# Performance work log

Hardware: AMD Instinct MI355X
Metric: run time of the kernel (lower is better)

The kernel has to match this reference:

```python
import jax, jax.numpy as jnp
import numpy as np

NSAMPLE = 16   # knn neighbors for cost volume
KCLUST = 8     # cluster size stand-in for custom_cluster_pc1 (min_count=8)
B, N, D = 2, 4096, 64


def _sqdist(src, dst):
    # src [B,N,C], dst [B,M,C] -> [B,N,M]
    d = (jnp.sum(src * src, -1)[:, :, None]
         + jnp.sum(dst * dst, -1)[:, None, :]
         - 2.0 * jnp.einsum('bnc,bmc->bnm', src, dst))
    return jnp.maximum(d, 0.0)


def _knn(k, xyz, new_xyz):
    return jax.lax.top_k(-_sqdist(new_xyz, xyz), k)[1]  # [B,S,k] indices of k smallest


def _group(points, idx):
    # points [B,M,C], idx [B,N,K] -> [B,N,K,C]
    b = jnp.arange(points.shape[0])[:, None, None]
    return points[b, idx]


def _weightnet(x, w1, b1, w2, b2, w3, b3):
    # x [B,N,K,3]; 1x1 conv stack == per-point MLP, relu
    h = jax.nn.relu(jnp.einsum('bnkc,cd->bnkd', x, w1) + b1)
    h = jax.nn.relu(jnp.einsum('bnkc,cd->bnkd', h, w2) + b2)
    return jax.nn.relu(jnp.einsum('bnkc,cd->bnkd', h, w3) + b3)


def _leaky(x):
    return jnp.where(x > 0, x, 0.1 * x)


def _forward(xyz1, xyz2, points1, points2, vel1, vel2, mask1, mask2,
             w_xyz, w_vel, w_points,
             mlp_w1, mlp_b1, mlp_w2, mlp_b2,
             wn1_w1, wn1_b1, wn1_w2, wn1_b2, wn1_w3, wn1_b3,
             wn2_w1, wn2_b1, wn2_w2, wn2_b2, wn2_w3, wn2_b3):
    xyz1t = jnp.transpose(xyz1, (0, 2, 1))      # [B,N1,3]
    xyz2t = jnp.transpose(xyz2, (0, 2, 1))      # [B,N2,3]
    p1t = jnp.transpose(points1, (0, 2, 1))     # [B,N1,D1]
    p2t = jnp.transpose(points2, (0, 2, 1))     # [B,N2,D2]

    # --- custom_cluster_pc1 stand-in: knn clusters of pc1 with its velocities ---
    idx_c = _knn(KCLUST, xyz1t, xyz1t)                     # [B,N,KC]
    cc = _group(xyz1t, idx_c)                              # [B,N,KC,3]
    cv = _group(vel1[..., None], idx_c)[..., 0]            # [B,N,KC]

    u = cc / jnp.linalg.norm(cc, axis=-1, keepdims=True)
    ATA = jnp.einsum('bnki,bnkj->bnij', u, u) + 1e-6 * jnp.eye(3, dtype=u.dtype)
    ATb = jnp.einsum('bnki,bnk->bni', u, cv)
    v_world = jnp.linalg.solve(ATA, ATb[..., None])[..., 0]  # [B,N,3]

    # --- feature-space knn between weighted (xyz, points) concatenations ---
    f1 = jnp.concatenate([w_xyz * xyz1t, w_points * p1t], axis=-1)
    f2 = jnp.concatenate([w_xyz * xyz2t, w_points * p2t], axis=-1)
    knn_idx = _knn(NSAMPLE, f2, f1)                        # [B,N1,K]

    neighbor_xyz = _group(xyz2t, knn_idx)                  # [B,N1,K,3]
    direction_xyz = neighbor_xyz - xyz1t[:, :, None, :]
    g2 = _group(p2t, knn_idx)                              # [B,N1,K,D2]
    g1 = jnp.broadcast_to(p1t[:, :, None, :], g2.shape[:3] + (p1t.shape[-1],))
    new_points = jnp.concatenate([g1, g2, direction_xyz], axis=-1)  # [B,N1,K,D1+D2+3]

    h = _leaky(jnp.einsum('bnkc,cd->bnkd', new_points, mlp_w1) + mlp_b1)
    h = _leaky(jnp.einsum('bnkc,cd->bnkd', h, mlp_w2) + mlp_b2)    # [B,N1,K,128]

    w = _weightnet(direction_xyz, wn1_w1, wn1_b1, wn1_w2, wn1_b2, wn1_w3, wn1_b3)
    point_to_patch = jnp.sum(w * h, axis=2)                # [B,N1,128]

    # --- second grouping in rigid-velocity space ---
    idx2 = _knn(NSAMPLE, v_world, v_world)
    nxyz1 = _group(xyz1t, idx2)
    dir2 = nxyz1 - xyz1t[:, :, None, :]
    w2 = _weightnet(dir2, wn2_w1, wn2_b1, wn2_w2, wn2_b2, wn2_w3, wn2_b3)
    gcost = _group(point_to_patch, idx2)                   # [B,N1,K,128]
    patch_to_patch = jnp.sum(w2 * gcost, axis=2)           # [B,N1,128]

    return jnp.transpose(patch_to_patch, (0, 2, 1)), v_world  # [B,128,N1], [B,N1,3]


def setup_inputs() -> dict:
    key = jax.random.key(0)
    ks = jax.random.split(key, 24)
    s = 0.05
    inp = {
        'xyz1': jax.random.normal(ks[0], (B, 3, N), jnp.float32),
        'xyz2': jax.random.normal(ks[1], (B, 3, N), jnp.float32),
        'points1': jax.random.normal(ks[2], (B, D, N), jnp.float32),
        'points2': jax.random.normal(ks[3], (B, D, N), jnp.float32),
        'vel1': jax.random.normal(ks[4], (B, N), jnp.float32),
        'vel2': jax.random.normal(ks[5], (B, N), jnp.float32),
        'mask1': jnp.ones((B, N), jnp.float32),
        'mask2': jnp.ones((B, N), jnp.float32),
        'w_xyz': jnp.float32(0.4), 'w_vel': jnp.float32(0.2), 'w_points': jnp.float32(0.4),
        'mlp_w1': jax.random.normal(ks[6], (2 * D + 3, 128), jnp.float32) * s,
        'mlp_b1': jnp.zeros((128,), jnp.float32),
        'mlp_w2': jax.random.normal(ks[7], (128, 128), jnp.float32) * s,
        'mlp_b2': jnp.zeros((128,), jnp.float32),
    }
    for tag, base in (('wn1', 8), ('wn2', 14)):
        inp[f'{tag}_w1'] = jax.random.normal(ks[base], (3, 8), jnp.float32) * s
        inp[f'{tag}_b1'] = jnp.zeros((8,), jnp.float32)
        inp[f'{tag}_w2'] = jax.random.normal(ks[base + 1], (8, 8), jnp.float32) * s
        inp[f'{tag}_b2'] = jnp.zeros((8,), jnp.float32)
        inp[f'{tag}_w3'] = jax.random.normal(ks[base + 2], (8, 128), jnp.float32) * s
        inp[f'{tag}_b3'] = jnp.zeros((128,), jnp.float32)
    return inp


def reference(xyz1, xyz2, points1, points2, vel1, vel2, mask1, mask2,
              w_xyz, w_vel, w_points,
              mlp_w1, mlp_b1, mlp_w2, mlp_b2,
              wn1_w1, wn1_b1, wn1_w2, wn1_b2, wn1_w3, wn1_b3,
              wn2_w1, wn2_b1, wn2_w2, wn2_b2, wn2_w3, wn2_b3):
    return _forward(xyz1, xyz2, points1, points2, vel1, vel2, mask1, mask2,
                    w_xyz, w_vel, w_points,
                    mlp_w1, mlp_b1, mlp_w2, mlp_b2,
                    wn1_w1, wn1_b1, wn1_w2, wn1_b2, wn1_w3, wn1_b3,
                    wn2_w1, wn2_b1, wn2_w2, wn2_b2, wn2_w3, wn2_b3)
```

## Files before the change

### kernel.cpp

```cpp
#include <hip/hip_runtime.h>

#define NPTS 4096
#define NQ   8192
#define DD   64
#define KNN  16
#define KC   8
#define NSEG 16
#define SEGLEN 256
#define KB96 96
#define VOFF 1048576

#define ALWAYS_INLINE __attribute__((always_inline)) inline

typedef __attribute__((ext_vector_type(8))) short bf16x8;
typedef __attribute__((ext_vector_type(4))) float f32x4;

__device__ ALWAYS_INLINE float leakyf(float x) { return x > 0.f ? x : 0.1f * x; }

__device__ ALWAYS_INLINE unsigned short bf16rne(float f) {
  unsigned u = __float_as_uint(f);
  u = (u + 0x7FFFu + ((u >> 16) & 1u)) >> 16;
  return (unsigned short)u;
}

__device__ ALWAYS_INLINE float packdt(float d, unsigned tag12) {
  return __uint_as_float((__float_as_uint(d) & 0xFFFFF000u) | tag12);
}

#define TK8_FOREACH(M)  M(0) M(1) M(2) M(3) M(4) M(5) M(6) M(7)
#define TK16_FOREACH(M) M(0) M(1) M(2) M(3) M(4) M(5) M(6) M(7) \
                        M(8) M(9) M(10) M(11) M(12) M(13) M(14) M(15)

#define TK_DECL1(i) float tkd##i = 3.4e38f; int tki##i = 0;
#define TK_STEP1(i) { bool c = vd < tkd##i; float t_ = tkd##i; int u_ = tki##i; \
                      tkd##i = c ? vd : tkd##i; tki##i = c ? vi : tki##i; \
                      vd = c ? t_ : vd; vi = c ? u_ : vi; }
#define TK8_DECL  TK8_FOREACH(TK_DECL1)
#define TK8_INS(dexp, mexp)  { float vd = (dexp); int vi = (mexp); \
                               if (vd < tkd7)  { TK8_FOREACH(TK_STEP1) } }

#define PK_DECL1(i) float pk##i = __uint_as_float(0x7F7FFFFFu);
#define PK_STEP1(i) { float lo_ = fminf(pk##i, pv); pv = fmaxf(pk##i, pv); pk##i = lo_; }
#define PK16_DECL    TK16_FOREACH(PK_DECL1)
#define PK16_INS(ve) { float pv = (ve); TK16_FOREACH(PK_STEP1) }
#define PK_STORE1(i) pdq[i] = pk##i;
#define PK16_STORE   TK16_FOREACH(PK_STORE1)

__global__ __launch_bounds__(256) void k_prep(
    const float* __restrict__ xyz1, const float* __restrict__ xyz2,
    const float* __restrict__ pts1, const float* __restrict__ pts2,
    const float* __restrict__ w_xyz_p, const float* __restrict__ w_points_p,
    unsigned short* __restrict__ f1b, unsigned short* __restrict__ f2b,
    float* __restrict__ n1, float* __restrict__ n2a,
    float* __restrict__ p1t, float* __restrict__ p2t,
    float* __restrict__ x1t, float* __restrict__ x2t)
{
  int gid = blockIdx.x * 256 + threadIdx.x;
  int b = gid >> 12, n = gid & (NPTS - 1);
  float wx = w_xyz_p[0], wp = w_points_p[0];
  {
    const float* xb = xyz1 + (size_t)b * 3 * NPTS;
    float x = xb[n], y = xb[NPTS + n], z = xb[2 * NPTS + n];
    float nrm2 = fmaf(z, z, fmaf(y, y, x * x));
    float4 xv; xv.x = x; xv.y = y; xv.z = z; xv.w = nrm2;
    *(float4*)&x1t[(size_t)gid * 4] = xv;
    float fx = wx * x, fy = wx * y, fz = wx * z;
    float acc = fmaf(fz, fz, fmaf(fy, fy, fx * fx));
    unsigned short* fr = f1b + (size_t)gid * KB96;
    fr[0] = bf16rne(fx); fr[1] = bf16rne(fy); fr[2] = bf16rne(fz);
    const float* pb = pts1 + (size_t)b * DD * NPTS;
    float* pr = p1t + (size_t)gid * DD;
    for (int c = 0; c < DD; ++c) {
      float v = pb[(size_t)c * NPTS + n];
      pr[c] = v;
      float fv = wp * v;
      fr[3 + c] = bf16rne(fv);
      acc = fmaf(fv, fv, acc);
    }
    for (int c = 67; c < KB96; ++c) fr[c] = 0;
    n1[gid] = acc;
  }
  {
    const float* xb = xyz2 + (size_t)b * 3 * NPTS;
    float x = xb[n], y = xb[NPTS + n], z = xb[2 * NPTS + n];
    float nrm2 = fmaf(z, z, fmaf(y, y, x * x));
    float4 xv; xv.x = x; xv.y = y; xv.z = z; xv.w = nrm2;
    *(float4*)&x2t[(size_t)gid * 4] = xv;
    float fx = wx * x, fy = wx * y, fz = wx * z;
    float acc = fmaf(fz, fz, fmaf(fy, fy, fx * fx));
    unsigned short* fr = f2b + (size_t)gid * KB96;
    fr[0] = bf16rne(fx); fr[1] = bf16rne(fy); fr[2] = bf16rne(fz);
    const float* pb = pts2 + (size_t)b * DD * NPTS;
    float* pr = p2t + (size_t)gid * DD;
    for (int c = 0; c < DD; ++c) {
      float v = pb[(size_t)c * NPTS + n];
      pr[c] = v;
      float fv = wp * v;
      fr[3 + c] = bf16rne(fv);
      acc = fmaf(fv, fv, acc);
    }
    for (int c = 67; c < KB96; ++c) fr[c] = 0;
    n2a[gid] = acc;
  }
}

__global__ __launch_bounds__(256) void k_knn3(
    const float* __restrict__ x4, float* __restrict__ pd, int* __restrict__ pi)
{
  __shared__ __align__(16) float4 sc[128];
  int seg = blockIdx.y;
  int Q = blockIdx.x * 256 + threadIdx.x;
  int b = Q >> 12;
  float4 q = *(const float4*)&x4[(size_t)Q * 4];
  TK8_DECL
  int gbase = (b << 12) + seg * SEGLEN;
  for (int ch = 0; ch < SEGLEN / 128; ++ch) {
    __syncthreads();
    if (threadIdx.x < 128)
      sc[threadIdx.x] = *(const float4*)&x4[(size_t)(gbase + ch * 128 + threadIdx.x) * 4];
    __syncthreads();
    int m0 = seg * SEGLEN + ch * 128;
    for (int j = 0; j < 128; ++j) {
      float4 c = sc[j];
      float dot = fmaf(q.z, c.z, fmaf(q.y, c.y, q.x * c.x));
      float d = fmaxf(q.w + c.w - 2.f * dot, 0.f);
      TK8_INS(d, m0 + j)
    }
  }
  float* pdq = pd + ((size_t)Q * NSEG + seg) * 16;
  int* piq = pi + ((size_t)Q * NSEG + seg) * 16;
#define ST8(i) pdq[i] = tkd##i; piq[i] = tki##i;
  TK8_FOREACH(ST8)
#undef ST8
}

__global__ __launch_bounds__(256) void k_knnv(
    const float* __restrict__ x4, float* __restrict__ pd)
{
  __shared__ __align__(16) float4 sc[128];
  int seg = blockIdx.y;
  int Q = blockIdx.x * 256 + threadIdx.x;
  int b = Q >> 12;
  float4 q = *(const float4*)&x4[(size_t)Q * 4];
  PK16_DECL
  int gbase = (b << 12) + seg * SEGLEN;
  for (int ch = 0; ch < SEGLEN / 128; ++ch) {
    __syncthreads();
    if (threadIdx.x < 128)
      sc[threadIdx.x] = *(const float4*)&x4[(size_t)(gbase + ch * 128 + threadIdx.x) * 4];
    __syncthreads();
    unsigned base_tag = ((unsigned)ch << 11) | (unsigned)seg;
#pragma unroll
    for (int j = 0; j < 128; ++j) {
      float4 c = sc[j];
      float dot = fmaf(q.z, c.z, fmaf(q.y, c.y, q.x * c.x));
      float d = fmaxf(q.w + c.w - 2.f * dot, 0.f);
      PK16_INS(packdt(d, base_tag | ((unsigned)j << 4)))
    }
  }
  float* pdq = pd + ((size_t)Q * NSEG + seg) * 16;
  PK16_STORE
}

__global__ __launch_bounds__(256) void k_rigid(
    const float* __restrict__ pd, const int* __restrict__ pi,
    const float* __restrict__ x4, const float* __restrict__ vel1,
    float* __restrict__ vout, float* __restrict__ v4out)
{
  int Q = blockIdx.x * 256 + threadIdx.x;
  int b = Q >> 12;
  TK8_DECL
  for (int s = 0; s < NSEG; ++s) {
    const float* pdq = pd + ((size_t)Q * NSEG + s) * 16;
    const int* piq = pi + ((size_t)Q * NSEG + s) * 16;
#pragma unroll
    for (int j = 0; j < KC; ++j) TK8_INS(pdq[j], piq[j])
  }
  int base = b << 12;
  double a00 = 0, a01 = 0, a02 = 0, a11 = 0, a12 = 0, a22 = 0;
  double r0 = 0, r1 = 0, r2 = 0;
#define RIG_ACC(i) { \
    float4 c = *(const float4*)&x4[(size_t)(base + tki##i) * 4]; \
    float nr = sqrtf(c.w); \
    float ux = c.x / nr, uy = c.y / nr, uz = c.z / nr; \
    float cv = vel1[base + tki##i]; \
    double dx = ux, dy = uy, dz = uz, dvv = cv; \
    a00 += dx * dx; a01 += dx * dy; a02 += dx * dz; \
    a11 += dy * dy; a12 += dy * dz; a22 += dz * dz; \
    r0 += dx * dvv; r1 += dy * dvv; r2 += dz * dvv; }
  TK8_FOREACH(RIG_ACC)
#undef RIG_ACC
  a00 += 1e-6; a11 += 1e-6; a22 += 1e-6;
  double c00 = a11 * a22 - a12 * a12;
  double c01 = a02 * a12 - a01 * a22;
  double c02 = a01 * a12 - a02 * a11;
  double c11 = a00 * a22 - a02 * a02;
  double c12 = a02 * a01 - a00 * a12;
  double c22 = a00 * a11 - a01 * a01;
  double det = a00 * c00 + a01 * c01 + a02 * c02;
  double inv = 1.0 / det;
  float vx = (float)((c00 * r0 + c01 * r1 + c02 * r2) * inv);
  float vy = (float)((c01 * r0 + c11 * r1 + c12 * r2) * inv);
  float vz = (float)((c02 * r0 + c12 * r1 + c22 * r2) * inv);
  vout[(size_t)Q * 3 + 0] = vx;
  vout[(size_t)Q * 3 + 1] = vy;
  vout[(size_t)Q * 3 + 2] = vz;
  float4 v; v.x = vx; v.y = vy; v.z = vz;
  v.w = fmaf(vz, vz, fmaf(vy, vy, vx * vx));
  *(float4*)&v4out[(size_t)Q * 4] = v;
}

__global__ __launch_bounds__(256) void k_knnf_mfma(
    const unsigned short* __restrict__ f1b, const unsigned short* __restrict__ f2b,
    const float* __restrict__ n1, const float* __restrict__ n2a,
    float* __restrict__ pd)
{
  __shared__ __align__(16) unsigned short sf1[16 * KB96];
  __shared__ __align__(16) unsigned short sf2[64 * KB96];
  __shared__ __align__(16) float sn1[16];
  __shared__ __align__(16) float sn2[64];
  __shared__ __align__(16) float sD[64][21];
  int tid = threadIdx.x;
  int w = tid >> 6, lane = tid & 63;
  int i15 = lane & 15, g = lane >> 4, kr0 = g * 8;
  int blockq = blockIdx.x * 16;
  int b = blockq >> 12;
  int seg = blockIdx.y;
  int gbase = (b << 12) + seg * 1024;
  {
    const float4* src = (const float4*)(f1b + (size_t)blockq * KB96);
    if (tid < 192) ((float4*)sf1)[tid] = src[tid];
    if (tid < 16) sn1[tid] = n1[blockq + tid];
  }
  __syncthreads();
  bf16x8 af0 = *(const bf16x8*)&sf1[i15 * KB96 + kr0];
  bf16x8 af1 = *(const bf16x8*)&sf1[i15 * KB96 + 32 + kr0];
  bf16x8 af2 = *(const bf16x8*)&sf1[i15 * KB96 + 64 + kr0];
  float nq0 = sn1[g * 4 + 0], nq1 = sn1[g * 4 + 1];
  float nq2 = sn1[g * 4 + 2], nq3 = sn1[g * 4 + 3];
  PK16_DECL
  int q_tk = tid & 15, p_tk = tid >> 4;
  for (int ch = 0; ch < 16; ++ch) {
    __syncthreads();
    {
      const float4* src = (const float4*)(f2b + (size_t)(gbase + ch * 64) * KB96);
      ((float4*)sf2)[tid] = src[tid];
      ((float4*)sf2)[tid + 256] = src[tid + 256];
      ((float4*)sf2)[tid + 512] = src[tid + 512];
      if (tid < 64) sn2[tid] = n2a[gbase + ch * 64 + tid];
    }
    __syncthreads();
    {
      int crow = w * 16 + i15;
      const unsigned short* c_ = &sf2[crow * KB96 + kr0];
      f32x4 acc = {0.f, 0.f, 0.f, 0.f};
      acc = __builtin_amdgcn_mfma_f32_16x16x32_bf16(af0, *(const bf16x8*)&c_[0],  acc, 0, 0, 0);
      acc = __builtin_amdgcn_mfma_f32_16x16x32_bf16(af1, *(const bf16x8*)&c_[32], acc, 0, 0, 0);
      acc = __builtin_amdgcn_mfma_f32_16x16x32_bf16(af2, *(const bf16x8*)&c_[64], acc, 0, 0, 0);
      float nn2 = sn2[crow];
      unsigned tag = (((unsigned)(ch * 16 + i15)) << 4) | (unsigned)(seg * 4 + w);
      sD[crow][g * 4 + 0] = packdt(fmaxf(nq0 + nn2 - 2.f * acc[0], 0.f), tag);
      sD[crow][g * 4 + 1] = packdt(fmaxf(nq1 + nn2 - 2.f * acc[1], 0.f), tag);
      sD[crow][g * 4 + 2] = packdt(fmaxf(nq2 + nn2 - 2.f * acc[2], 0.f), tag);
      sD[crow][g * 4 + 3] = packdt(fmaxf(nq3 + nn2 - 2.f * acc[3], 0.f), tag);
    }
    __syncthreads();
    if (tid < 64) {
#pragma unroll
      for (int cl = 0; cl < 16; ++cl)
        PK16_INS(sD[p_tk * 16 + cl][q_tk])
    }
  }
  if (tid < 64) {
    int pseg = seg * 4 + p_tk;
    float* pdq = pd + ((size_t)(blockq + q_tk) * NSEG + pseg) * 16;
    PK16_STORE
  }
}

template<int MODE>
__global__ __launch_bounds__(256) void k_mergepk(
    const float* __restrict__ pd, int* __restrict__ oidx)
{
  int Q = blockIdx.x * 256 + threadIdx.x;
  PK16_DECL
  for (int s = 0; s < NSEG; ++s) {
    const float* pdq = pd + ((size_t)Q * NSEG + s) * 16;
    for (int j = 0; j < 16; ++j) {
      float v = pdq[j];
      if (__all(!(v < pk15))) break;
      PK16_INS(v)
    }
  }
#define DEC(i) { unsigned u = __float_as_uint(pk##i); int m_; \
    if (MODE == 0) { unsigned ps = u & 15u, lo = (u >> 4) & 255u; \
      m_ = (int)(((ps >> 2) << 10) + ((lo >> 4) << 6) + ((ps & 3u) << 4) + (lo & 15u)); } \
    else { m_ = (int)(((u & 15u) << 8) + ((u >> 4) & 255u)); } \
    oidx[(size_t)Q * KNN + i] = m_; }
  TK16_FOREACH(DEC)
#undef DEC
}

#define PPB 8
__device__ ALWAYS_INLINE bf16x8 load_wfrag(const float* __restrict__ Wg,
                                           int kbase, int col, int kmax) {
  bf16x8 r;
#pragma unroll
  for (int j = 0; j < 8; ++j) {
    int k = kbase + j;
    float f = (k < kmax) ? Wg[(size_t)k * 128 + col] : 0.f;
    r[j] = (short)bf16rne(f);
  }
  return r;
}

__global__ __launch_bounds__(512) void k_mlp_mfma(
    const float* __restrict__ p1t, const float* __restrict__ p2t,
    const float* __restrict__ x1t, const float* __restrict__ x2t,
    const int* __restrict__ kidx,
    const float* __restrict__ W1, const float* __restrict__ B1v,
    const float* __restrict__ W2, const float* __restrict__ B2v,
    const float* __restrict__ wnw1, const float* __restrict__ wnb1,
    const float* __restrict__ wnw2, const float* __restrict__ wnb2,
    const float* __restrict__ wnw3, const float* __restrict__ wnb3,
    float* __restrict__ ptp)
{
  __shared__ __align__(16) unsigned short sA1[16 * 168];
  __shared__ __align__(16) unsigned short sH1[16 * 136];
  __shared__ __align__(16) float s_wv[16 * 128];
  __shared__ __align__(16) float s_c1[24];
  __shared__ __align__(16) float s_cb1[8];
  __shared__ __align__(16) float s_c2[64];
  __shared__ __align__(16) float s_cb2[8];
  __shared__ __align__(16) float s_w3[1024];
  __shared__ __align__(16) float s_b3[128];
  int tid = threadIdx.x;
  int w = tid >> 6, lane = tid & 63;
  int col = (w << 4) + (lane & 15);
  int kr0 = (lane >> 4) * 8;
  if (tid < 24) s_c1[tid] = wnw1[tid];
  else if (tid < 32) s_cb1[tid - 24] = wnb1[tid - 24];
  else if (tid < 96) s_c2[tid - 32] = wnw2[tid - 32];
  else if (tid < 104) s_cb2[tid - 96] = wnb2[tid - 96];
  if (tid >= 128 && tid < 256) s_b3[tid - 128] = wnb3[tid - 128];
  for (int i = tid; i < 1024; i += 512) s_w3[i] = wnw3[i];
  bf16x8 w1f0 = load_wfrag(W1, 0 + kr0, col, 131);
  bf16x8 w1f1 = load_wfrag(W1, 32 + kr0, col, 131);
  bf16x8 w1f2 = load_wfrag(W1, 64 + kr0, col, 131);
  bf16x8 w1f3 = load_wfrag(W1, 96 + kr0, col, 131);
  bf16x8 w1f4 = load_wfrag(W1, 128 + kr0, col, 131);
  bf16x8 w2f0 = load_wfrag(W2, 0 + kr0, col, 128);
  bf16x8 w2f1 = load_wfrag(W2, 32 + kr0, col, 128);
  bf16x8 w2f2 = load_wfrag(W2, 64 + kr0, col, 128);
  bf16x8 w2f3 = load_wfrag(W2, 96 + kr0, col, 128);
  float b1c = B1v[col], b2c = B2v[col];
  int blk0 = blockIdx.x * PPB;
  int base = (blk0 >> 12) << 12;
  int r_st = tid >> 5, t_st = tid & 31;

  for (int p = 0; p < PPB; ++p) {
    int gid = blk0 + p;
    __syncthreads();
    {
      int m = kidx[(size_t)gid * 16 + r_st];
      int grow = base + m;
      float4 cx1 = *(const float4*)&x1t[(size_t)gid * 4];
      float4 cx2 = *(const float4*)&x2t[(size_t)grow * 4];
      unsigned short* row = &sA1[r_st * 168];
      row[t_st]      = bf16rne(p1t[(size_t)gid * 64 + t_st]);
      row[t_st + 32] = bf16rne(p1t[(size_t)gid * 64 + t_st + 32]);
      row[t_st + 64] = bf16rne(p2t[(size_t)grow * 64 + t_st]);
      row[t_st + 96] = bf16rne(p2t[(size_t)grow * 64 + t_st + 32]);
      float dx = cx2.x - cx1.x, dy = cx2.y - cx1.y, dz = cx2.z - cx1.z;
      float dv_ = (t_st == 0) ? dx : (t_st == 1) ? dy : (t_st == 2) ? dz : 0.f;
      row[t_st + 128] = bf16rne(dv_);
      float h1w0 = fmaxf(fmaf(dz, s_c1[16], fmaf(dy, s_c1[8],  fmaf(dx, s_c1[0], s_cb1[0]))), 0.f);
      float h1w1 = fmaxf(fmaf(dz, s_c1[17], fmaf(dy, s_c1[9],  fmaf(dx, s_c1[1], s_cb1[1]))), 0.f);
      float h1w2 = fmaxf(fmaf(dz, s_c1[18], fmaf(dy, s_c1[10], fmaf(dx, s_c1[2], s_cb1[2]))), 0.f);
      float h1w3 = fmaxf(fmaf(dz, s_c1[19], fmaf(dy, s_c1[11], fmaf(dx, s_c1[3], s_cb1[3]))), 0.f);
      float h1w4 = fmaxf(fmaf(dz, s_c1[20], fmaf(dy, s_c1[12], fmaf(dx, s_c1[4], s_cb1[4]))), 0.f);
      float h1w5 = fmaxf(fmaf(dz, s_c1[21], fmaf(dy, s_c1[13], fmaf(dx, s_c1[5], s_cb1[5]))), 0.f);
      float h1w6 = fmaxf(fmaf(dz, s_c1[22], fmaf(dy, s_c1[14], fmaf(dx, s_c1[6], s_cb1[6]))), 0.f);
      float h1w7 = fmaxf(fmaf(dz, s_c1[23], fmaf(dy, s_c1[15], fmaf(dx, s_c1[7], s_cb1[7]))), 0.f);
#define H2W(j) float h2w##j; { float a_ = s_cb2[j]; \
      a_ = fmaf(h1w0, s_c2[0 * 8 + j], a_); a_ = fmaf(h1w1, s_c2[1 * 8 + j], a_); \
      a_ = fmaf(h1w2, s_c2[2 * 8 + j], a_); a_ = fmaf(h1w3, s_c2[3 * 8 + j], a_); \
      a_ = fmaf(h1w4, s_c2[4 * 8 + j], a_); a_ = fmaf(h1w5, s_c2[5 * 8 + j], a_); \
      a_ = fmaf(h1w6, s_c2[6 * 8 + j], a_); a_ = fmaf(h1w7, s_c2[7 * 8 + j], a_); \
      h2w##j = fmaxf(a_, 0.f); }
      H2W(0) H2W(1) H2W(2) H2W(3) H2W(4) H2W(5) H2W(6) H2W(7)
#undef H2W
      int c4 = t_st * 4;
      float4 wv = *(const float4*)&s_b3[c4];
#define WV(j) { float4 w3 = *(const float4*)&s_w3[j * 128 + c4]; \
      wv.x = fmaf(h2w##j, w3.x, wv.x); wv.y = fmaf(h2w##j, w3.y, wv.y); \
      wv.z = fmaf(h2w##j, w3.z, wv.z); wv.w = fmaf(h2w##j, w3.w, wv.w); }
      WV(0) WV(1) WV(2) WV(3) WV(4) WV(5) WV(6) WV(7)
#undef WV
      wv.x = fmaxf(wv.x, 0.f); wv.y = fmaxf(wv.y, 0.f);
      wv.z = fmaxf(wv.z, 0.f); wv.w = fmaxf(wv.w, 0.f);
      *(float4*)&s_wv[r_st * 128 + c4] = wv;
    }
    __syncthreads();
    {
      int ab = (lane & 15) * 168 + kr0;
      f32x4 acc = {0.f, 0.f, 0.f, 0.f};
      acc = __builtin_amdgcn_mfma_f32_16x16x32_bf16(*(const bf16x8*)&sA1[ab],       w1f0, acc, 0, 0, 0);
      acc = __builtin_amdgcn_mfma_f32_16x16x32_bf16(*(const bf16x8*)&sA1[ab + 32],  w1f1, acc, 0, 0, 0);
      acc = __builtin_amdgcn_mfma_f32_16x16x32_bf16(*(const bf16x8*)&sA1[ab + 64],  w1f2, acc, 0, 0, 0);
      acc = __builtin_amdgcn_mfma_f32_16x16x32_bf16(*(const bf16x8*)&sA1[ab + 96],  w1f3, acc, 0, 0, 0);
      acc = __builtin_amdgcn_mfma_f32_16x16x32_bf16(*(const bf16x8*)&sA1[ab + 128], w1f4, acc, 0, 0, 0);
      int rw0 = (lane >> 4) * 4;
#pragma unroll
      for (int r = 0; r < 4; ++r)
        sH1[(rw0 + r) * 136 + col] = bf16rne(leakyf(acc[r] + b1c));
    }
    __syncthreads();
    {
      int ab = (lane & 15) * 136 + kr0;
      f32x4 acc = {0.f, 0.f, 0.f, 0.f};
      acc = __builtin_amdgcn_mfma_f32_16x16x32_bf16(*(const bf16x8*)&sH1[ab],      w2f0, acc, 0, 0, 0);
      acc = __builtin_amdgcn_mfma_f32_16x16x32_bf16(*(const bf16x8*)&sH1[ab + 32], w2f1, acc, 0, 0, 0);
      acc = __builtin_amdgcn_mfma_f32_16x16x32_bf16(*(const bf16x8*)&sH1[ab + 64], w2f2, acc, 0, 0, 0);
      acc = __builtin_amdgcn_mfma_f32_16x16x32_bf16(*(const bf16x8*)&sH1[ab + 96], w2f3, acc, 0, 0, 0);
      int rw0 = (lane >> 4) * 4;
      float v = 0.f;
#pragma unroll
      for (int r = 0; r < 4; ++r)
        v = fmaf(s_wv[(rw0 + r) * 128 + col], leakyf(acc[r] + b2c), v);
      v += __shfl_xor(v, 16);
      v += __shfl_xor(v, 32);
      if (lane < 16) ptp[(size_t)gid * 128 + col] = v;
    }
  }
}

__global__ __launch_bounds__(256) void k_final(
    const float* __restrict__ x1t, const int* __restrict__ idx2,
    const float* __restrict__ ptp,
    const float* __restrict__ wnw1, const float* __restrict__ wnb1,
    const float* __restrict__ wnw2, const float* __restrict__ wnb2,
    const float* __restrict__ wnw3, const float* __restrict__ wnb3,
    float* __restrict__ out0)
{
  __shared__ __align__(16) float s_gc[16][128];
  __shared__ __align__(16) float s_wn[16][8];
  __shared__ __align__(16) float s_red[2][128];
  int gid = blockIdx.x, b = gid >> 12, n = gid & (NPTS - 1);
  int tid = threadIdx.x;
  if (tid < 16) {
    int m = idx2[(size_t)gid * 16 + tid];
    float4 c2 = *(const float4*)&x1t[(size_t)((b << 12) + m) * 4];
    float4 c1 = *(const float4*)&x1t[(size_t)gid * 4];
    float dx = c2.x - c1.x, dy = c2.y - c1.y, dz = c2.z - c1.z;
    float h1w[8];
#pragma unroll
    for (int j = 0; j < 8; ++j)
      h1w[j] = fmaxf(fmaf(dz, wnw1[16 + j], fmaf(dy, wnw1[8 + j], fmaf(dx, wnw1[j], wnb1[j]))), 0.f);
#pragma unroll
    for (int j = 0; j < 8; ++j) {
      float a = wnb2[j];
#pragma unroll
      for (int qq = 0; qq < 8; ++qq) a = fmaf(h1w[qq], wnw2[qq * 8 + j], a);
      s_wn[tid][j] = fmaxf(a, 0.f);
    }
  }
  int k2 = tid >> 4, i2 = tid & 15;
  int mg = idx2[(size_t)gid * 16 + k2];
  const float* src = &ptp[(size_t)((b << 12) + mg) * 128 + i2 * 8];
  *(float4*)&s_gc[k2][i2 * 8] = *(const float4*)&src[0];
  *(float4*)&s_gc[k2][i2 * 8 + 4] = *(const float4*)&src[4];
  __syncthreads();
  int ch = tid & 127, kg2 = tid >> 7;
  float r = 0.f;
#pragma unroll
  for (int jj = 0; jj < 8; ++jj) {
    int k = kg2 * 8 + jj;
    float4 wa = *(const float4*)&s_wn[k][0];
    float4 wb = *(const float4*)&s_wn[k][4];
    float wv = wnb3[ch];
    wv = fmaf(wa.x, wnw3[ch], wv);
    wv = fmaf(wa.y, wnw3[128 + ch], wv);
    wv = fmaf(wa.z, wnw3[256 + ch], wv);
    wv = fmaf(wa.w, wnw3[384 + ch], wv);
    wv = fmaf(wb.x, wnw3[512 + ch], wv);
    wv = fmaf(wb.y, wnw3[640 + ch], wv);
    wv = fmaf(wb.z, wnw3[768 + ch], wv);
    wv = fmaf(wb.w, wnw3[896 + ch], wv);
    wv = fmaxf(wv, 0.f);
    r = fmaf(wv, s_gc[k][ch], r);
  }
  s_red[kg2][ch] = r;
  __syncthreads();
  if (tid < 128)
    out0[(size_t)(b * 128 + tid) * NPTS + n] = s_red[0][tid] + s_red[1][tid];
}

extern "C" void kernel_launch(void* const* d_in, const int* in_sizes, int n_in,
                              void* d_out, int out_size, void* d_ws, size_t ws_size,
                              hipStream_t stream) {
  (void)in_sizes; (void)n_in; (void)out_size; (void)ws_size;
  const float* xyz1   = (const float*)d_in[0];
  const float* xyz2   = (const float*)d_in[1];
  const float* pts1   = (const float*)d_in[2];
  const float* pts2   = (const float*)d_in[3];
  const float* vel1   = (const float*)d_in[4];
  const float* w_xyz  = (const float*)d_in[8];
  const float* w_pts  = (const float*)d_in[10];
  const float* mlp_w1 = (const float*)d_in[11];
  const float* mlp_b1 = (const float*)d_in[12];
  const float* mlp_w2 = (const float*)d_in[13];
  const float* mlp_b2 = (const float*)d_in[14];
  const float* wn1_w1 = (const float*)d_in[15];
  const float* wn1_b1 = (const float*)d_in[16];
  const float* wn1_w2 = (const float*)d_in[17];
  const float* wn1_b2 = (const float*)d_in[18];
  const float* wn1_w3 = (const float*)d_in[19];
  const float* wn1_b3 = (const float*)d_in[20];
  const float* wn2_w1 = (const float*)d_in[21];
  const float* wn2_b1 = (const float*)d_in[22];
  const float* wn2_w2 = (const float*)d_in[23];
  const float* wn2_b2 = (const float*)d_in[24];
  const float* wn2_w3 = (const float*)d_in[25];
  const float* wn2_b3 = (const float*)d_in[26];

  char* ws = (char*)d_ws;
  size_t off = 0;
  float* pd   = (float*)(ws + off); off += (size_t)NQ * NSEG * 16 * 4;
  int*   pi   = (int*)(ws + off);   off += (size_t)NQ * NSEG * 16 * 4;
  unsigned short* f1b = (unsigned short*)(ws + off); off += (size_t)NQ * KB96 * 2;
  unsigned short* f2b = (unsigned short*)(ws + off); off += (size_t)NQ * KB96 * 2;
  float* n1   = (float*)(ws + off); off += (size_t)NQ * 4;
  float* n2a  = (float*)(ws + off); off += (size_t)NQ * 4;
  float* p1t  = (float*)(ws + off); off += (size_t)NQ * DD * 4;
  float* p2t  = (float*)(ws + off); off += (size_t)NQ * DD * 4;
  float* x1t  = (float*)(ws + off); off += (size_t)NQ * 4 * 4;
  float* x2t  = (float*)(ws + off); off += (size_t)NQ * 4 * 4;
  int*   kidx = (int*)(ws + off);   off += (size_t)NQ * KNN * 4;
  float* ptp  = (float*)(ws + off); off += (size_t)NQ * 128 * 4;
  int*   idx2 = (int*)(ws + off);   off += (size_t)NQ * KNN * 4;
  float* v4   = (float*)(ws + off); off += (size_t)NQ * 4 * 4;

  float* out0 = (float*)d_out;
  float* outv = (float*)d_out + VOFF;

  k_prep<<<32, 256, 0, stream>>>(xyz1, xyz2, pts1, pts2, w_xyz, w_pts,
                                 f1b, f2b, n1, n2a, p1t, p2t, x1t, x2t);
  k_knn3<<<dim3(32, NSEG), 256, 0, stream>>>(x1t, pd, pi);
  k_rigid<<<32, 256, 0, stream>>>(pd, pi, x1t, vel1, outv, v4);
  k_knnf_mfma<<<dim3(NQ / 16, 4), 256, 0, stream>>>(f1b, f2b, n1, n2a, pd);
  k_mergepk<0><<<32, 256, 0, stream>>>(pd, kidx);
  k_mlp_mfma<<<NQ / PPB, 512, 0, stream>>>(p1t, p2t, x1t, x2t, kidx,
                                           mlp_w1, mlp_b1, mlp_w2, mlp_b2,
                                           wn1_w1, wn1_b1, wn1_w2, wn1_b2,
                                           wn1_w3, wn1_b3, ptp);
  k_knnv<<<dim3(32, NSEG), 256, 0, stream>>>(v4, pd);
  k_mergepk<1><<<32, 256, 0, stream>>>(pd, idx2);
  k_final<<<NQ, 256, 0, stream>>>(x1t, idx2, ptp,
                                  wn2_w1, wn2_b1, wn2_w2, wn2_b2, wn2_w3, wn2_b3, out0);
}
```

Measured before the change: 380.7 us.

## Parallelize top-k across all threads with 32 partial segments and padded LDS

```diff
diff --git a/kernel.cpp b/kernel.cpp
--- a/kernel.cpp
+++ b/kernel.cpp
@@ -6,8 +6,10 @@
 #define KNN  16
 #define KC   8
 #define NSEG 16
+#define NPSEG 32
 #define SEGLEN 256
 #define KB96 96
+#define FSTR 104
 #define VOFF 1048576
 
 #define ALWAYS_INLINE __attribute__((always_inline)) inline
@@ -143,22 +145,18 @@
   int b = Q >> 12;
   float4 q = *(const float4*)&x4[(size_t)Q * 4];
   PK16_DECL
-  int gbase = (b << 12) + seg * SEGLEN;
-  for (int ch = 0; ch < SEGLEN / 128; ++ch) {
-    __syncthreads();
-    if (threadIdx.x < 128)
-      sc[threadIdx.x] = *(const float4*)&x4[(size_t)(gbase + ch * 128 + threadIdx.x) * 4];
-    __syncthreads();
-    unsigned base_tag = ((unsigned)ch << 11) | (unsigned)seg;
-#pragma unroll
-    for (int j = 0; j < 128; ++j) {
-      float4 c = sc[j];
-      float dot = fmaf(q.z, c.z, fmaf(q.y, c.y, q.x * c.x));
-      float d = fmaxf(q.w + c.w - 2.f * dot, 0.f);
-      PK16_INS(packdt(d, base_tag | ((unsigned)j << 4)))
-    }
-  }
-  float* pdq = pd + ((size_t)Q * NSEG + seg) * 16;
+  int gbase = (b << 12) + seg * 128;
+  if (threadIdx.x < 128)
+    sc[threadIdx.x] = *(const float4*)&x4[(size_t)(gbase + threadIdx.x) * 4];
+  __syncthreads();
+#pragma unroll
+  for (int j = 0; j < 128; ++j) {
+    float4 c = sc[j];
+    float dot = fmaf(q.z, c.z, fmaf(q.y, c.y, q.x * c.x));
+    float d = fmaxf(q.w + c.w - 2.f * dot, 0.f);
+    PK16_INS(packdt(d, ((unsigned)j << 5) | (unsigned)seg))
+  }
+  float* pdq = pd + ((size_t)Q * NPSEG + seg) * 16;
   PK16_STORE
 }
 
@@ -215,67 +213,65 @@
     const float* __restrict__ n1, const float* __restrict__ n2a,
     float* __restrict__ pd)
 {
-  __shared__ __align__(16) unsigned short sf1[16 * KB96];
-  __shared__ __align__(16) unsigned short sf2[64 * KB96];
+  __shared__ __align__(16) unsigned short sf1[16 * FSTR];
+  __shared__ __align__(16) unsigned short sf2[64 * FSTR];
   __shared__ __align__(16) float sn1[16];
   __shared__ __align__(16) float sn2[64];
-  __shared__ __align__(16) float sD[64][21];
+  __shared__ __align__(16) float sD[64][17];
   int tid = threadIdx.x;
   int w = tid >> 6, lane = tid & 63;
   int i15 = lane & 15, g = lane >> 4, kr0 = g * 8;
   int blockq = blockIdx.x * 16;
   int b = blockq >> 12;
   int seg = blockIdx.y;
-  int gbase = (b << 12) + seg * 1024;
+  int gbase = (b << 12) + seg * 2048;
   {
     const float4* src = (const float4*)(f1b + (size_t)blockq * KB96);
-    if (tid < 192) ((float4*)sf1)[tid] = src[tid];
+    if (tid < 192) ((float4*)sf1)[tid + tid / 12] = src[tid];
     if (tid < 16) sn1[tid] = n1[blockq + tid];
   }
   __syncthreads();
-  bf16x8 af0 = *(const bf16x8*)&sf1[i15 * KB96 + kr0];
-  bf16x8 af1 = *(const bf16x8*)&sf1[i15 * KB96 + 32 + kr0];
-  bf16x8 af2 = *(const bf16x8*)&sf1[i15 * KB96 + 64 + kr0];
+  bf16x8 af0 = *(const bf16x8*)&sf1[i15 * FSTR + kr0];
+  bf16x8 af1 = *(const bf16x8*)&sf1[i15 * FSTR + 32 + kr0];
+  bf16x8 af2 = *(const bf16x8*)&sf1[i15 * FSTR + 64 + kr0];
   float nq0 = sn1[g * 4 + 0], nq1 = sn1[g * 4 + 1];
   float nq2 = sn1[g * 4 + 2], nq3 = sn1[g * 4 + 3];
   PK16_DECL
   int q_tk = tid & 15, p_tk = tid >> 4;
-  for (int ch = 0; ch < 16; ++ch) {
+  for (int ch = 0; ch < 32; ++ch) {
     __syncthreads();
     {
       const float4* src = (const float4*)(f2b + (size_t)(gbase + ch * 64) * KB96);
-      ((float4*)sf2)[tid] = src[tid];
-      ((float4*)sf2)[tid + 256] = src[tid + 256];
-      ((float4*)sf2)[tid + 512] = src[tid + 512];
+      int i0 = tid, i1 = tid + 256, i2 = tid + 512;
+      ((float4*)sf2)[i0 + i0 / 12] = src[i0];
+      ((float4*)sf2)[i1 + i1 / 12] = src[i1];
+      ((float4*)sf2)[i2 + i2 / 12] = src[i2];
       if (tid < 64) sn2[tid] = n2a[gbase + ch * 64 + tid];
     }
     __syncthreads();
     {
       int crow = w * 16 + i15;
-      const unsigned short* c_ = &sf2[crow * KB96 + kr0];
+      const unsigned short* c_ = &sf2[crow * FSTR + kr0];
       f32x4 acc = {0.f, 0.f, 0.f, 0.f};
       acc = __builtin_amdgcn_mfma_f32_16x16x32_bf16(af0, *(const bf16x8*)&c_[0],  acc, 0, 0, 0);
       acc = __builtin_amdgcn_mfma_f32_16x16x32_bf16(af1, *(const bf16x8*)&c_[32], acc, 0, 0, 0);
       acc = __builtin_amdgcn_mfma_f32_16x16x32_bf16(af2, *(const bf16x8*)&c_[64], acc, 0, 0, 0);
       float nn2 = sn2[crow];
-      unsigned tag = (((unsigned)(ch * 16 + i15)) << 4) | (unsigned)(seg * 4 + w);
+      unsigned tag = (((unsigned)(ch * 4 + (crow & 3))) << 5) |
+                     (unsigned)(seg * 16 + (crow >> 2));
       sD[crow][g * 4 + 0] = packdt(fmaxf(nq0 + nn2 - 2.f * acc[0], 0.f), tag);
       sD[crow][g * 4 + 1] = packdt(fmaxf(nq1 + nn2 - 2.f * acc[1], 0.f), tag);
       sD[crow][g * 4 + 2] = packdt(fmaxf(nq2 + nn2 - 2.f * acc[2], 0.f), tag);
       sD[crow][g * 4 + 3] = packdt(fmaxf(nq3 + nn2 - 2.f * acc[3], 0.f), tag);
     }
     __syncthreads();
-    if (tid < 64) {
-#pragma unroll
-      for (int cl = 0; cl < 16; ++cl)
-        PK16_INS(sD[p_tk * 16 + cl][q_tk])
-    }
-  }
-  if (tid < 64) {
-    int pseg = seg * 4 + p_tk;
-    float* pdq = pd + ((size_t)(blockq + q_tk) * NSEG + pseg) * 16;
-    PK16_STORE
-  }
+#pragma unroll
+    for (int j = 0; j < 4; ++j)
+      PK16_INS(sD[p_tk * 4 + j][q_tk])
+  }
+  int pseg = seg * 16 + p_tk;
+  float* pdq = pd + ((size_t)(blockq + q_tk) * NPSEG + pseg) * 16;
+  PK16_STORE
 }
 
 template<int MODE>
@@ -284,8 +280,8 @@
 {
   int Q = blockIdx.x * 256 + threadIdx.x;
   PK16_DECL
-  for (int s = 0; s < NSEG; ++s) {
-    const float* pdq = pd + ((size_t)Q * NSEG + s) * 16;
+  for (int s = 0; s < NPSEG; ++s) {
+    const float* pdq = pd + ((size_t)Q * NPSEG + s) * 16;
     for (int j = 0; j < 16; ++j) {
       float v = pdq[j];
       if (__all(!(v < pk15))) break;
@@ -293,9 +289,9 @@
     }
   }
 #define DEC(i) { unsigned u = __float_as_uint(pk##i); int m_; \
-    if (MODE == 0) { unsigned ps = u & 15u, lo = (u >> 4) & 255u; \
-      m_ = (int)(((ps >> 2) << 10) + ((lo >> 4) << 6) + ((ps & 3u) << 4) + (lo & 15u)); } \
-    else { m_ = (int)(((u & 15u) << 8) + ((u >> 4) & 255u)); } \
+    unsigned ps = u & 31u, lo = (u >> 5) & 127u; \
+    if (MODE == 0) m_ = (int)(((ps >> 4) << 11) + ((lo >> 2) << 6) + ((ps & 15u) << 2) + (lo & 3u)); \
+    else m_ = (int)((ps << 7) + lo); \
     oidx[(size_t)Q * KNN + i] = m_; }
   TK16_FOREACH(DEC)
 #undef DEC
@@ -526,7 +522,7 @@
 
   char* ws = (char*)d_ws;
   size_t off = 0;
-  float* pd   = (float*)(ws + off); off += (size_t)NQ * NSEG * 16 * 4;
+  float* pd   = (float*)(ws + off); off += (size_t)NQ * NPSEG * 16 * 4;
   int*   pi   = (int*)(ws + off);   off += (size_t)NQ * NSEG * 16 * 4;
   unsigned short* f1b = (unsigned short*)(ws + off); off += (size_t)NQ * KB96 * 2;
   unsigned short* f2b = (unsigned short*)(ws + off); off += (size_t)NQ * KB96 * 2;
@@ -548,13 +544,13 @@
                                  f1b, f2b, n1, n2a, p1t, p2t, x1t, x2t);
   k_knn3<<<dim3(32, NSEG), 256, 0, stream>>>(x1t, pd, pi);
   k_rigid<<<32, 256, 0, stream>>>(pd, pi, x1t, vel1, outv, v4);
-  k_knnf_mfma<<<dim3(NQ / 16, 4), 256, 0, stream>>>(f1b, f2b, n1, n2a, pd);
+  k_knnf_mfma<<<dim3(NQ / 16, 2), 256, 0, stream>>>(f1b, f2b, n1, n2a, pd);
   k_mergepk<0><<<32, 256, 0, stream>>>(pd, kidx);
   k_mlp_mfma<<<NQ / PPB, 512, 0, stream>>>(p1t, p2t, x1t, x2t, kidx,
                                            mlp_w1, mlp_b1, mlp_w2, mlp_b2,
                                            wn1_w1, wn1_b1, wn1_w2, wn1_b2,
                                            wn1_w3, wn1_b3, ptp);
-  k_knnv<<<dim3(32, NSEG), 256, 0, stream>>>(v4, pd);
+  k_knnv<<<dim3(32, 32), 256, 0, stream>>>(v4, pd);
   k_mergepk<1><<<32, 256, 0, stream>>>(pd, idx2);
   k_final<<<NQ, 256, 0, stream>>>(x1t, idx2, ptp,
                                   wn2_w1, wn2_b1, wn2_w2, wn2_b2, wn2_w3, wn2_b3, out0);
```

Measured after the change: 406.4 us. 1.07x slower.
